# Kernel optimization log

Measured on AMD Instinct MI355X. Metric: run time of the kernel, lower is better.

Reference implementation:

```python
import jax, jax.numpy as jnp
import numpy as np

B, DIM, H, W = 1, 96, 192, 192
HEADS = 6
HD = DIM // HEADS
WIN = (8, 4)
STRIDE = (4, 2)
WH, WW = WIN
N = WH * WW
SCALE = HD ** -0.5
EPS = 1e-8

_hs = np.arange(0, H - WH + 1, STRIDE[0])
_ws = np.arange(0, W - WW + 1, STRIDE[1])
NH, NW = len(_hs), len(_ws)
HIDX = jnp.asarray(_hs[:, None] + np.arange(WH)[None, :])  # (NH, WH)
WIDX = jnp.asarray(_ws[:, None] + np.arange(WW)[None, :])  # (NW, WW)

# relative-position index table (N, N)
_co = np.stack(np.meshgrid(np.arange(WH), np.arange(WW), indexing='ij')).reshape(2, -1)
_rp = _co[:, :, None] - _co[:, None, :]
_rp[0] += WH - 1
_rp[1] += WW - 1
_rp[0] *= 2 * WW - 1
REL_IDX = jnp.asarray(_rp[0] + _rp[1])


def _clin(wr, wi, x):
    # complex 1x1 conv as channel matmul
    xr, xi = x.real, x.imag
    yr = jnp.einsum('oc,nchw->nohw', wr, xr) - jnp.einsum('oc,nchw->nohw', wi, xi)
    yi = jnp.einsum('oc,nchw->nohw', wr, xi) + jnp.einsum('oc,nchw->nohw', wi, xr)
    return jax.lax.complex(yr, yi)


def _bn(x, g, b):
    # BatchNorm2d in training mode: batch statistics, biased variance, eps=1e-5
    mu = x.mean(axis=(0, 2, 3), keepdims=True)
    var = ((x - mu) ** 2).mean(axis=(0, 2, 3), keepdims=True)
    return g[None, :, None, None] * (x - mu) * jax.lax.rsqrt(var + 1e-5) + b[None, :, None, None]


def _cbn(x, gr, br, gi, bi):
    return jax.lax.complex(_bn(x.real, gr, br), _bn(x.imag, gi, bi))


def _cgelu(x):
    mag = jnp.abs(x)
    return x * (jax.nn.gelu(mag, approximate=False) / (mag + EPS))


def _heads(t):
    # (Bn, H*D, wh, ww) -> (Bn, H, N, D)
    return t.reshape(-1, HEADS, HD, N).transpose(0, 1, 3, 2)


def reference(x_real, x_imag, qkv_wr, qkv_wi, proj_wr, proj_wi, rel,
              mlp1_wr, mlp1_wi, mlp2_wr, mlp2_wi,
              n1_gr, n1_br, n1_gi, n1_bi, n2_gr, n2_br, n2_gi, n2_bi):
    x = jax.lax.complex(x_real, x_imag)  # (B, C, H, W)

    # unfold: gather overlapping windows -> (B, C, NH, NW, WH, WW)
    xw = x[:, :, HIDX[:, None, :, None], WIDX[None, :, None, :]]
    xw = xw.transpose(0, 2, 3, 1, 4, 5).reshape(B * NH * NW, DIM, WH, WW)

    qkv = _clin(qkv_wr, qkv_wi, xw)
    q, k, v = jnp.split(qkv, 3, axis=1)
    q, k, v = _heads(q), _heads(k), _heads(v)

    attn = jnp.einsum('bhnd,bhmd->bhnm', q, jnp.conj(k)) * SCALE
    bias = rel[:, REL_IDX]  # (HEADS, N, N), real
    attn = attn + bias[None]
    mag = jnp.abs(attn)
    wsm = jax.nn.softmax(mag, axis=-1)
    attn = attn * (wsm / (mag + EPS))  # magnitude-softmax, phase preserved
    out = jnp.einsum('bhnm,bhmd->bhnd', attn, v)
    out = out.transpose(0, 1, 3, 2).reshape(-1, DIM, WH, WW)
    out = _clin(proj_wr, proj_wi, out)

    # fold: scatter-add windows back, then overlap-average
    out = out.reshape(B, NH, NW, DIM, WH, WW).transpose(0, 3, 1, 2, 4, 5)
    folded = jnp.zeros((B, DIM, H, W), jnp.complex64).at[
        :, :, HIDX[:, None, :, None], WIDX[None, :, None, :]].add(out)
    counts = jnp.zeros((H, W), jnp.float32).at[
        HIDX[:, None, :, None], WIDX[None, :, None, :]].add(1.0)
    x_ = folded / (counts + EPS)

    x = _cbn(x + x_, n1_gr, n1_br, n1_gi, n1_bi)
    m = _clin(mlp2_wr, mlp2_wi, _cgelu(_clin(mlp1_wr, mlp1_wi, x)))
    x = _cbn(x + m, n2_gr, n2_br, n2_gi, n2_bi)
    return jnp.stack([x.real, x.imag], axis=0)  # (2, B, C, H, W)


def setup_inputs() -> dict:
    key = jax.random.key(0)
    ks = jax.random.split(key, 11)
    n = lambda k, s: jax.random.normal(k, s, jnp.float32) * 0.02
    return {
        'x_real': jax.random.normal(ks[0], (B, DIM, H, W), jnp.float32),
        'x_imag': jax.random.normal(ks[1], (B, DIM, H, W), jnp.float32),
        'qkv_wr': n(ks[2], (3 * DIM, DIM)), 'qkv_wi': n(ks[3], (3 * DIM, DIM)),
        'proj_wr': n(ks[4], (DIM, DIM)), 'proj_wi': n(ks[5], (DIM, DIM)),
        'rel': n(ks[6], (HEADS, (2 * WH - 1) * (2 * WW - 1))),
        'mlp1_wr': n(ks[7], (4 * DIM, DIM)), 'mlp1_wi': n(ks[8], (4 * DIM, DIM)),
        'mlp2_wr': n(ks[9], (DIM, 4 * DIM)), 'mlp2_wi': n(ks[10], (DIM, 4 * DIM)),
        'n1_gr': jnp.ones(DIM), 'n1_br': jnp.zeros(DIM),
        'n1_gi': jnp.ones(DIM), 'n1_bi': jnp.zeros(DIM),
        'n2_gr': jnp.ones(DIM), 'n2_br': jnp.zeros(DIM),
        'n2_gi': jnp.ones(DIM), 'n2_bi': jnp.zeros(DIM),
    }
```

## Files before the change

### kernel.cpp

```cpp
#include <hip/hip_runtime.h>
#include <hip/hip_bf16.h>
#include <math.h>

#define PIX 36864
#define IMW 192
#define NWIN 4465
#define NWIN_W 95
#define NTASK (NWIN * 6)

typedef short bf16x8 __attribute__((ext_vector_type(8)));
typedef short bf16x4 __attribute__((ext_vector_type(4)));
typedef float floatx4 __attribute__((ext_vector_type(4)));

#if defined(__has_builtin)
#  if __has_builtin(__builtin_amdgcn_rcpf)
#    define RCP(x) __builtin_amdgcn_rcpf(x)
#  endif
#endif
#ifndef RCP
#  define RCP(x) (1.0f / (x))
#endif

__device__ __forceinline__ unsigned short f2bf(float f) {
    __hip_bfloat16 h = __float2bfloat16(f);
    return __builtin_bit_cast(unsigned short, h);
}
__device__ __forceinline__ float bf2f(unsigned short b) {
    union { unsigned u; float f; } v; v.u = ((unsigned)b) << 16;
    return v.f;
}

__device__ __forceinline__ void emit3(
    const float* __restrict__ wr, const float* __restrict__ wi,
    unsigned short* __restrict__ outr, unsigned short* __restrict__ outi,
    unsigned short* __restrict__ outni, int e)
{
    outr[e] = f2bf(wr[e]);
    unsigned short b = f2bf(wi[e]);
    outi[e]  = b;
    outni[e] = b ^ 0x8000;
}

__global__ __launch_bounds__(256) void prep_kernel(
    const float* __restrict__ qwr, const float* __restrict__ qwi,
    const float* __restrict__ pwr, const float* __restrict__ pwi,
    const float* __restrict__ w2r, const float* __restrict__ w2i,
    const float* __restrict__ xr,  const float* __restrict__ xi,
    unsigned short* __restrict__ wq, unsigned short* __restrict__ wp,
    unsigned short* __restrict__ w2, float* __restrict__ ssum,
    unsigned short* __restrict__ dr, unsigned short* __restrict__ di)
{
    int blk = blockIdx.x;
    if (blk < 108)      { emit3(qwr, qwi, wq, wq + 27648, wq + 55296, blk * 256 + threadIdx.x); return; }
    if (blk < 144)      { emit3(pwr, pwi, wp, wp + 9216,  wp + 18432, (blk - 108) * 256 + threadIdx.x); return; }
    if (blk < 288)      { emit3(w2r, w2i, w2, w2 + 36864, w2 + 73728, (blk - 144) * 256 + threadIdx.x); return; }
    if (blk == 288)     { for (int j = threadIdx.x; j < 768; j += 256) ssum[j] = 0.f; return; }
    int e  = blk - 289;
    int kb = e / 144;
    int n  = (e % 144) * 256 + threadIdx.x;
    bf16x8 vr, vi;
#pragma unroll
    for (int j = 0; j < 8; ++j) {
        ((unsigned short*)&vr)[j] = f2bf(xr[(size_t)(kb * 8 + j) * PIX + n]);
        ((unsigned short*)&vi)[j] = f2bf(xi[(size_t)(kb * 8 + j) * PIX + n]);
    }
    *(bf16x8*)&dr[((size_t)kb * PIX + n) * 8] = vr;
    *(bf16x8*)&di[((size_t)kb * PIX + n) * 8] = vi;
}

template<int K, int MT, int STORE>
__global__ __launch_bounds__(256, 2) void cgemm_mfma_kernel(
    const unsigned short* __restrict__ Wr, const unsigned short* __restrict__ Wi,
    const unsigned short* __restrict__ Wni,
    const unsigned short* __restrict__ Xr, const unsigned short* __restrict__ Xi,
    unsigned short* __restrict__ Pr, unsigned short* __restrict__ Pi, int N)
{
    const int lane = threadIdx.x & 63;
    const int wave = threadIdx.x >> 6;
    const int g = lane >> 4;
    const int r = lane & 15;
    const int m0 = (blockIdx.x % MT) * 32;
    const int n0 = (blockIdx.x / MT) * 256 + wave * 64;

    floatx4 accR[2][4], accI[2][4];
#pragma unroll
    for (int t = 0; t < 2; ++t)
#pragma unroll
        for (int j = 0; j < 4; ++j) {
            accR[t][j] = (floatx4){0.f, 0.f, 0.f, 0.f};
            accI[t][j] = (floatx4){0.f, 0.f, 0.f, 0.f};
        }

    for (int kc = 0; kc < K; kc += 32) {
        bf16x8 awr[2], awi[2], awni[2];
#pragma unroll
        for (int t = 0; t < 2; ++t) {
            size_t wb = (size_t)(m0 + t * 16 + r) * K + kc + g * 8;
            awr[t]  = *(const bf16x8*)&Wr[wb];
            awi[t]  = *(const bf16x8*)&Wi[wb];
            awni[t] = *(const bf16x8*)&Wni[wb];
        }
        bf16x8 bxr[4], bxi[4];
        const size_t krow = (size_t)((kc >> 3) + g);
#pragma unroll
        for (int j = 0; j < 4; ++j) {
            size_t off = (krow * N + n0 + j * 16 + r) * 8;
            bxr[j] = *(const bf16x8*)&Xr[off];
            bxi[j] = *(const bf16x8*)&Xi[off];
        }
#pragma unroll
        for (int t = 0; t < 2; ++t)
#pragma unroll
            for (int j = 0; j < 4; ++j) {
                accR[t][j] = __builtin_amdgcn_mfma_f32_16x16x32_bf16(awr[t],  bxr[j], accR[t][j], 0, 0, 0);
                accR[t][j] = __builtin_amdgcn_mfma_f32_16x16x32_bf16(awni[t], bxi[j], accR[t][j], 0, 0, 0);
                accI[t][j] = __builtin_amdgcn_mfma_f32_16x16x32_bf16(awr[t],  bxi[j], accI[t][j], 0, 0, 0);
                accI[t][j] = __builtin_amdgcn_mfma_f32_16x16x32_bf16(awi[t],  bxr[j], accI[t][j], 0, 0, 0);
            }
    }

    if (STORE == 3) {
#pragma unroll
        for (int t = 0; t < 2; ++t)
#pragma unroll
            for (int j = 0; j < 4; ++j) {
                int col = n0 + j * 16 + r;
#pragma unroll
                for (int reg = 0; reg < 4; ++reg) {
                    int row = m0 + t * 16 + g * 4 + reg;
                    Pr[(size_t)row * N + col] = f2bf(accR[t][j][reg]);
                    Pi[(size_t)row * N + col] = f2bf(accI[t][j][reg]);
                }
            }
    } else {
#pragma unroll
        for (int t = 0; t < 2; ++t) {
            int ch0 = m0 + t * 16;
            int which = ch0 / 96;
            int hh = (ch0 % 96) / 16;
#pragma unroll
            for (int j = 0; j < 4; ++j) {
                int col = n0 + j * 16 + r;
                bf16x4 pr, pi;
#pragma unroll
                for (int reg = 0; reg < 4; ++reg) {
                    ((unsigned short*)&pr)[reg] = f2bf(accR[t][j][reg]);
                    ((unsigned short*)&pi)[reg] = f2bf(accI[t][j][reg]);
                }
                size_t sb = (((size_t)col * 3 + which) * 6 + hh) * 32;
                *(bf16x4*)&Pr[sb + g * 4]      = pr;
                *(bf16x4*)&Pr[sb + 16 + g * 4] = pi;
            }
        }
    }
}

__global__ __launch_bounds__(256) void attn_mfma_kernel(
    const unsigned short* __restrict__ qkvb,
    const float* __restrict__ rel,
    unsigned short* __restrict__ wout)
{
    __shared__ unsigned aLDS[4][32 * 36];
    __shared__ unsigned vLDS[4][32 * 17];

    const int wv   = threadIdx.x >> 6;
    const int lane = threadIdx.x & 63;
    const int lr   = lane & 15;
    const int g    = lane >> 4;

    int t = blockIdx.x * 4 + wv;
    if (t >= NTASK) t = NTASK - 1;
    const int w = t / 6, h = t % 6;
    const int nh = w / NWIN_W, nw = w % NWIN_W;
    const int r0 = nh * 4, c0 = nw * 2;
    const int slot = ((nh & 1) << 1) | (nw & 1);

    unsigned* AL = aLDS[wv];
    unsigned* VL = vLDS[wv];

    auto slotq = [&](int p, int which) -> size_t {
        int gpix = (r0 + (p >> 2)) * IMW + c0 + (p & 3);
        return ((size_t)gpix * 18 + which * 6 + h) * 32;
    };

    {
        int m = lane & 31;
        int half = lane >> 5;
        size_t sv = slotq(m, 2);
        const bf16x8 vr = *(const bf16x8*)&qkvb[sv + half * 8];
        const bf16x8 vi = *(const bf16x8*)&qkvb[sv + 16 + half * 8];
#pragma unroll
        for (int j = 0; j < 8; ++j) {
            unsigned pk = (unsigned)(unsigned short)vr[j] |
                          ((unsigned)(unsigned short)vi[j] << 16);
            VL[m * 17 + half * 8 + j] = pk;
        }
    }

    const int hoff = (g >> 1) * 16;
    const int loff = (g & 1) * 8;
    const unsigned sm = (g >= 2) ? 0x80008000u : 0u;
    bf16x8 Are[2], Aim[2], Bre[2], Bim[2];
#pragma unroll
    for (int tt = 0; tt < 2; ++tt) {
        size_t sq = slotq(tt * 16 + lr, 0);
        size_t sk = slotq(tt * 16 + lr, 1);
        Are[tt] = *(const bf16x8*)&qkvb[sq + hoff + loff];
        Aim[tt] = *(const bf16x8*)&qkvb[sq + (16 - hoff) + loff];
        Bre[tt] = *(const bf16x8*)&qkvb[sk + hoff + loff];
        bf16x8 tmp = Bre[tt];
        unsigned* u = (unsigned*)&tmp;
        u[0] ^= sm; u[1] ^= sm; u[2] ^= sm; u[3] ^= sm;
        Bim[tt] = tmp;
    }

    const floatx4 z4 = (floatx4){0.f, 0.f, 0.f, 0.f};
    floatx4 Sre[2][2], Sim[2][2];
#pragma unroll
    for (int tn = 0; tn < 2; ++tn)
#pragma unroll
        for (int tm = 0; tm < 2; ++tm) {
            Sre[tn][tm] = __builtin_amdgcn_mfma_f32_16x16x32_bf16(Are[tn], Bre[tm], z4, 0, 0, 0);
            Sim[tn][tm] = __builtin_amdgcn_mfma_f32_16x16x32_bf16(Aim[tn], Bim[tm], z4, 0, 0, 0);
        }

    const float* relh = rel + h * 105;
#pragma unroll
    for (int tn = 0; tn < 2; ++tn)
#pragma unroll
        for (int tm = 0; tm < 2; ++tm) {
            int m = tm * 16 + lr;
            int ym = m >> 2, xm = m & 3;
            int yn = tn * 4 + g;
            int bidx = (yn - ym + 7) * 7 + (3 - xm);
#pragma unroll
            for (int reg = 0; reg < 4; ++reg) {
                float re = Sre[tn][tm][reg] * 0.25f + relh[bidx + reg];
                float im = Sim[tn][tm][reg] * 0.25f;
                int n = tn * 16 + g * 4 + reg;
                AL[n * 36 + m] = (unsigned)f2bf(re) | ((unsigned)f2bf(im) << 16);
            }
        }
    __syncthreads();

    {
        const int row = lane & 31;
        const int half = lane >> 5;
        unsigned* rp = &AL[row * 36 + half * 16];
        unsigned pk[16];
        *(uint4*)&pk[0]  = *(const uint4*)&rp[0];
        *(uint4*)&pk[4]  = *(const uint4*)&rp[4];
        *(uint4*)&pk[8]  = *(const uint4*)&rp[8];
        *(uint4*)&pk[12] = *(const uint4*)&rp[12];
        float re[16], im[16], mg[16], rr[16];
#pragma unroll
        for (int j = 0; j < 16; ++j) {
            union { unsigned u; float f; } a, b;
            a.u = pk[j] << 16;
            b.u = pk[j] & 0xffff0000u;
            re[j] = a.f; im[j] = b.f;
            float m2 = fmaf(a.f, a.f, b.f * b.f);
            float rv = rsqrtf(m2 + 1e-16f);
            rr[j] = rv;
            mg[j] = m2 * rv;
        }
        float mx = mg[0];
#pragma unroll
        for (int j = 1; j < 16; ++j) mx = fmaxf(mx, mg[j]);
        mx = fmaxf(mx, __shfl_xor(mx, 32, 64));
        float es[16], ss = 0.f;
#pragma unroll
        for (int j = 0; j < 16; ++j) { es[j] = __expf(mg[j] - mx); ss += es[j]; }
        ss += __shfl_xor(ss, 32, 64);
        float inv = RCP(ss);
#pragma unroll
        for (int j = 0; j < 16; ++j) {
            float f = es[j] * inv * rr[j];
            pk[j] = (unsigned)f2bf(re[j] * f) | ((unsigned)f2bf(im[j] * f) << 16);
        }
        *(uint4*)&rp[0]  = *(uint4*)&pk[0];
        *(uint4*)&rp[4]  = *(uint4*)&pk[4];
        *(uint4*)&rp[8]  = *(uint4*)&pk[8];
        *(uint4*)&rp[12] = *(uint4*)&pk[12];
    }
    __syncthreads();

    floatx4 Pre[2] = {z4, z4}, Pim[2] = {z4, z4};
#pragma unroll
    for (int kc = 0; kc < 2; ++kc) {
        bf16x8 Bpr, Bpi;
        unsigned* bpr = (unsigned*)&Bpr;
        unsigned* bpi = (unsigned*)&Bpi;
#pragma unroll
        for (int p = 0; p < 4; ++p) {
            unsigned pv = VL[(kc * 16 + g * 4 + p) * 17 + lr];
            bpr[p] = pv ^ 0x80000000u;
            bpi[p] = (pv >> 16) | (pv << 16);
        }
#pragma unroll
        for (int tn = 0; tn < 2; ++tn) {
            bf16x8 Af = *(bf16x8*)&AL[(tn * 16 + lr) * 36 + kc * 16 + g * 4];
            Pre[tn] = __builtin_amdgcn_mfma_f32_16x16x32_bf16(Af, Bpr, Pre[tn], 0, 0, 0);
            Pim[tn] = __builtin_amdgcn_mfma_f32_16x16x32_bf16(Af, Bpi, Pim[tn], 0, 0, 0);
        }
    }

#pragma unroll
    for (int tn = 0; tn < 2; ++tn)
#pragma unroll
        for (int reg = 0; reg < 4; ++reg) {
            int n = tn * 16 + g * 4 + reg;
            int gpix = (r0 + (n >> 2)) * IMW + c0 + (n & 3);
            int ch = h * 16 + lr;
            unsigned pk = (unsigned)f2bf(Pre[tn][reg]) |
                          ((unsigned)f2bf(Pim[tn][reg]) << 16);
            *(unsigned*)&wout[(((size_t)gpix * 4 + slot) * 96 + ch) * 2] = pk;
        }
}

__global__ __launch_bounds__(256) void fold_pack_kernel(
    const unsigned short* __restrict__ wout,
    unsigned short* __restrict__ dr, unsigned short* __restrict__ di)
{
    int e = blockIdx.x * 256 + threadIdx.x;
    int gpix = e / 12;
    int kb   = e % 12;
    int r = gpix / IMW, c = gpix % IMW;
    int nh0 = (r >= 7) ? ((r - 4) >> 2) : 0;
    int nh1 = min(46, r >> 2);
    int nw0 = (c >= 3) ? ((c - 2) >> 1) : 0;
    int nw1 = min(94, c >> 1);

    float accr[8] = {0,0,0,0,0,0,0,0}, acci[8] = {0,0,0,0,0,0,0,0};
    int cnt = 0;
    for (int nh = nh0; nh <= nh1; ++nh)
        for (int nw = nw0; nw <= nw1; ++nw) {
            int slot = ((nh & 1) << 1) | (nw & 1);
            const unsigned short* src = &wout[(((size_t)gpix * 4 + slot) * 96 + kb * 8) * 2];
            bf16x8 a = *(const bf16x8*)&src[0];
            bf16x8 b = *(const bf16x8*)&src[8];
#pragma unroll
            for (int j = 0; j < 4; ++j) {
                accr[j]     += bf2f((unsigned short)a[j*2]);
                acci[j]     += bf2f((unsigned short)a[j*2+1]);
                accr[4 + j] += bf2f((unsigned short)b[j*2]);
                acci[4 + j] += bf2f((unsigned short)b[j*2+1]);
            }
            ++cnt;
        }
    float invc = 1.0f / ((float)cnt + 1e-8f);
    bf16x8 pr, pi;
#pragma unroll
    for (int j = 0; j < 8; ++j) {
        ((unsigned short*)&pr)[j] = f2bf(accr[j] * invc);
        ((unsigned short*)&pi)[j] = f2bf(acci[j] * invc);
    }
    *(bf16x8*)&dr[((size_t)kb * PIX + gpix) * 8] = pr;
    *(bf16x8*)&di[((size_t)kb * PIX + gpix) * 8] = pi;
}

__device__ __forceinline__ void reduce32_commit(
    float* st, int kb, float* __restrict__ ssum)
{
#pragma unroll
    for (int v = 0; v < 32; ++v)
#pragma unroll
        for (int msk = 1; msk < 64; msk <<= 1)
            st[v] += __shfl_xor(st[v], msk, 64);
    __shared__ float red[4][32];
    const int wv = threadIdx.x >> 6;
    if ((threadIdx.x & 63) == 0)
#pragma unroll
        for (int v = 0; v < 32; ++v) red[wv][v] = st[v];
    __syncthreads();
    if (threadIdx.x < 32) {
        float s = red[0][threadIdx.x] + red[1][threadIdx.x] +
                  red[2][threadIdx.x] + red[3][threadIdx.x];
        int ch = kb * 8 + (threadIdx.x >> 2);
        int stat = threadIdx.x & 3;
        int base = (stat < 2) ? ch : 96 + ch;
        atomicAdd(&ssum[base * 2 + (stat & 1)], s);
    }
}

__global__ __launch_bounds__(256) void combine_pack_kernel(
    const float* __restrict__ xr, const float* __restrict__ xi,
    const unsigned short* __restrict__ pr, const unsigned short* __restrict__ pi,
    unsigned short* __restrict__ dr, unsigned short* __restrict__ di,
    float* __restrict__ ssum)
{
    const int kb = blockIdx.x / 36;
    const int pb = blockIdx.x % 36;
    const int p0 = pb * 1024;
    float st[32];
#pragma unroll
    for (int v = 0; v < 32; ++v) st[v] = 0.f;

#pragma unroll
    for (int it = 0; it < 4; ++it) {
        int p = p0 + it * 256 + threadIdx.x;
        bf16x8 vr, vi;
#pragma unroll
        for (int ch = 0; ch < 8; ++ch) {
            int c = kb * 8 + ch;
            float a = xr[(size_t)c * PIX + p] + bf2f(pr[(size_t)c * PIX + p]);
            float b = xi[(size_t)c * PIX + p] + bf2f(pi[(size_t)c * PIX + p]);
            ((unsigned short*)&vr)[ch] = f2bf(a);
            ((unsigned short*)&vi)[ch] = f2bf(b);
            st[ch * 4 + 0] += a; st[ch * 4 + 1] += a * a;
            st[ch * 4 + 2] += b; st[ch * 4 + 3] += b * b;
        }
        *(bf16x8*)&dr[((size_t)kb * PIX + p) * 8] = vr;
        *(bf16x8*)&di[((size_t)kb * PIX + p) * 8] = vi;
    }
    reduce32_commit(st, kb, ssum);
}

__global__ __launch_bounds__(256) void scale_w_kernel(
    const float* __restrict__ w1r, const float* __restrict__ w1i,
    const float* __restrict__ gr, const float* __restrict__ br,
    const float* __restrict__ gi, const float* __restrict__ bi,
    const float* __restrict__ ssum1,
    unsigned short* __restrict__ W0, unsigned short* __restrict__ W1,
    unsigned short* __restrict__ W2, unsigned short* __restrict__ W3,
    float* __restrict__ biasR, float* __restrict__ biasI)
{
    const float invn = 1.0f / (float)PIX;
    int blk = blockIdx.x;
    if (blk < 576) {
        int e = blk * 256 + threadIdx.x;
        int mat = e / 36864;
        int idx = e % 36864;
        int k = idx % 96;
        float mr = ssum1[k * 2] * invn;
        float a_r = gr[k] * rsqrtf(ssum1[k * 2 + 1] * invn - mr * mr + 1e-5f);
        float mi = ssum1[(96 + k) * 2] * invn;
        float a_i = gi[k] * rsqrtf(ssum1[(96 + k) * 2 + 1] * invn - mi * mi + 1e-5f);
        float wr = w1r[idx], wi = w1i[idx];
        float v = (mat == 0) ? wr * a_r : (mat == 1) ? -wi * a_i
                : (mat == 2) ? wr * a_i : wi * a_r;
        unsigned short* dst = (mat == 0) ? W0 : (mat == 1) ? W1 : (mat == 2) ? W2 : W3;
        dst[idx] = f2bf(v);
    } else {
        int o = (blk - 576) * 256 + threadIdx.x;
        if (o >= 768) return;
        int isI = o >= 384;
        int oo = o % 384;
        float acc = 0.f;
        for (int k = 0; k < 96; ++k) {
            float mr = ssum1[k * 2] * invn;
            float a_r = gr[k] * rsqrtf(ssum1[k * 2 + 1] * invn - mr * mr + 1e-5f);
            float c_r = br[k] - a_r * mr;
            float mi = ssum1[(96 + k) * 2] * invn;
            float a_i = gi[k] * rsqrtf(ssum1[(96 + k) * 2 + 1] * invn - mi * mi + 1e-5f);
            float c_i = bi[k] - a_i * mi;
            float wr = w1r[oo * 96 + k], wi = w1i[oo * 96 + k];
            acc += isI ? (wr * c_i + wi * c_r) : (wr * c_r - wi * c_i);
        }
        (isI ? biasI : biasR)[oo] = acc;
    }
}

__global__ __launch_bounds__(256, 2) void mlp1bn_kernel(
    const unsigned short* __restrict__ W0, const unsigned short* __restrict__ W1,
    const unsigned short* __restrict__ W2, const unsigned short* __restrict__ W3,
    const float* __restrict__ biasR, const float* __restrict__ biasI,
    const unsigned short* __restrict__ Xr, const unsigned short* __restrict__ Xi,
    unsigned short* __restrict__ Pr, unsigned short* __restrict__ Pi, int N)
{
    const int lane = threadIdx.x & 63;
    const int wave = threadIdx.x >> 6;
    const int g = lane >> 4;
    const int r = lane & 15;
    const int m0 = (blockIdx.x % 12) * 32;
    const int n0 = (blockIdx.x / 12) * 256 + wave * 64;
    const int K = 96;

    floatx4 accR[2][4], accI[2][4];
#pragma unroll
    for (int t = 0; t < 2; ++t)
#pragma unroll
        for (int j = 0; j < 4; ++j) {
            accR[t][j] = (floatx4){0.f, 0.f, 0.f, 0.f};
            accI[t][j] = (floatx4){0.f, 0.f, 0.f, 0.f};
        }

    for (int kc = 0; kc < K; kc += 32) {
        bf16x8 a0[2], a1[2], a2[2], a3[2];
#pragma unroll
        for (int t = 0; t < 2; ++t) {
            size_t wb = (size_t)(m0 + t * 16 + r) * K + kc + g * 8;
            a0[t] = *(const bf16x8*)&W0[wb];
            a1[t] = *(const bf16x8*)&W1[wb];
            a2[t] = *(const bf16x8*)&W2[wb];
            a3[t] = *(const bf16x8*)&W3[wb];
        }
        bf16x8 bxr[4], bxi[4];
        const size_t krow = (size_t)((kc >> 3) + g);
#pragma unroll
        for (int j = 0; j < 4; ++j) {
            size_t off = (krow * N + n0 + j * 16 + r) * 8;
            bxr[j] = *(const bf16x8*)&Xr[off];
            bxi[j] = *(const bf16x8*)&Xi[off];
        }
#pragma unroll
        for (int t = 0; t < 2; ++t)
#pragma unroll
            for (int j = 0; j < 4; ++j) {
                accR[t][j] = __builtin_amdgcn_mfma_f32_16x16x32_bf16(a0[t], bxr[j], accR[t][j], 0, 0, 0);
                accR[t][j] = __builtin_amdgcn_mfma_f32_16x16x32_bf16(a1[t], bxi[j], accR[t][j], 0, 0, 0);
                accI[t][j] = __builtin_amdgcn_mfma_f32_16x16x32_bf16(a2[t], bxi[j], accI[t][j], 0, 0, 0);
                accI[t][j] = __builtin_amdgcn_mfma_f32_16x16x32_bf16(a3[t], bxr[j], accI[t][j], 0, 0, 0);
            }
    }

#pragma unroll
    for (int t = 0; t < 2; ++t) {
        float bR[4], bI[4];
#pragma unroll
        for (int reg = 0; reg < 4; ++reg) {
            int row = m0 + t * 16 + g * 4 + reg;
            bR[reg] = biasR[row];
            bI[reg] = biasI[row];
        }
#pragma unroll
        for (int j = 0; j < 4; ++j) {
            int col = n0 + j * 16 + r;
            size_t rowblk = (size_t)((m0 + t * 16 + g * 4) >> 3);
            int sub = (g & 1) * 4;
            bf16x4 pr, pi;
#pragma unroll
            for (int reg = 0; reg < 4; ++reg) {
                float a = accR[t][j][reg] + bR[reg];
                float b = accI[t][j][reg] + bI[reg];
                float m2 = fmaf(a, a, b * b);
                float rv = rsqrtf(m2 + 1e-16f);
                float mag = m2 * rv;
                float f = (0.5f + 0.5f * erff(mag * 0.70710678118654752f)) * mag * rv;
                ((unsigned short*)&pr)[reg] = f2bf(a * f);
                ((unsigned short*)&pi)[reg] = f2bf(b * f);
            }
            *(bf16x4*)&Pr[(rowblk * N + col) * 8 + sub] = pr;
            *(bf16x4*)&Pi[(rowblk * N + col) * 8 + sub] = pi;
        }
    }
}

__global__ __launch_bounds__(256) void addbn_kernel(
    const unsigned short* __restrict__ dr, const unsigned short* __restrict__ di,
    const float* __restrict__ ssum1,
    const float* __restrict__ gr, const float* __restrict__ br,
    const float* __restrict__ gi, const float* __restrict__ bi,
    const unsigned short* __restrict__ mr_, const unsigned short* __restrict__ mi_,
    unsigned short* __restrict__ s2r, unsigned short* __restrict__ s2i,
    float* __restrict__ ssum2)
{
    const int kb = blockIdx.x / 36;
    const int pb = blockIdx.x % 36;
    const int p0 = pb * 1024;
    const float invn = 1.0f / (float)PIX;

    float ar[8], cr[8], ai[8], ci[8];
#pragma unroll
    for (int ch = 0; ch < 8; ++ch) {
        int c = kb * 8 + ch;
        float mr = ssum1[c * 2] * invn;
        ar[ch] = gr[c] * rsqrtf(ssum1[c * 2 + 1] * invn - mr * mr + 1e-5f);
        cr[ch] = br[c] - ar[ch] * mr;
        float mi = ssum1[(96 + c) * 2] * invn;
        ai[ch] = gi[c] * rsqrtf(ssum1[(96 + c) * 2 + 1] * invn - mi * mi + 1e-5f);
        ci[ch] = bi[c] - ai[ch] * mi;
    }

    float st[32];
#pragma unroll
    for (int v = 0; v < 32; ++v) st[v] = 0.f;

#pragma unroll
    for (int it = 0; it < 4; ++it) {
        int p = p0 + it * 256 + threadIdx.x;
        bf16x8 s1r = *(const bf16x8*)&dr[((size_t)kb * PIX + p) * 8];
        bf16x8 s1i = *(const bf16x8*)&di[((size_t)kb * PIX + p) * 8];
#pragma unroll
        for (int ch = 0; ch < 8; ++ch) {
            int c = kb * 8 + ch;
            float vr = bf2f(mr_[(size_t)c * PIX + p]) + ar[ch] * bf2f((unsigned short)s1r[ch]) + cr[ch];
            float vi = bf2f(mi_[(size_t)c * PIX + p]) + ai[ch] * bf2f((unsigned short)s1i[ch]) + ci[ch];
            s2r[(size_t)c * PIX + p] = f2bf(vr);
            s2i[(size_t)c * PIX + p] = f2bf(vi);
            st[ch * 4 + 0] += vr; st[ch * 4 + 1] += vr * vr;
            st[ch * 4 + 2] += vi; st[ch * 4 + 3] += vi * vi;
        }
    }
    reduce32_commit(st, kb, ssum2);
}

__global__ __launch_bounds__(256) void bn_apply_kernel(
    const unsigned short* __restrict__ s2r, const unsigned short* __restrict__ s2i,
    const float* __restrict__ gr, const float* __restrict__ br,
    const float* __restrict__ gi, const float* __restrict__ bi,
    const float* __restrict__ ssum2,
    float* __restrict__ outr, float* __restrict__ outi)
{
    int e = blockIdx.x * 256 + threadIdx.x;
    if (e >= 96 * PIX) return;
    int ch = e / PIX;
    const float invn = 1.0f / (float)PIX;
    float mr = ssum2[ch * 2] * invn;
    float isr = rsqrtf(ssum2[ch * 2 + 1] * invn - mr * mr + 1e-5f);
    float mi = ssum2[(96 + ch) * 2] * invn;
    float isi = rsqrtf(ssum2[(96 + ch) * 2 + 1] * invn - mi * mi + 1e-5f);
    outr[e] = gr[ch] * (bf2f(s2r[e]) - mr) * isr + br[ch];
    outi[e] = gi[ch] * (bf2f(s2i[e]) - mi) * isi + bi[ch];
}

extern "C" void kernel_launch(void* const* d_in, const int* in_sizes, int n_in,
                              void* d_out, int out_size, void* d_ws, size_t ws_size,
                              hipStream_t stream)
{
    const float* x_r     = (const float*)d_in[0];
    const float* x_i     = (const float*)d_in[1];
    const float* qkv_wr  = (const float*)d_in[2];
    const float* qkv_wi  = (const float*)d_in[3];
    const float* proj_wr = (const float*)d_in[4];
    const float* proj_wi = (const float*)d_in[5];
    const float* rel     = (const float*)d_in[6];
    const float* mlp1_wr = (const float*)d_in[7];
    const float* mlp1_wi = (const float*)d_in[8];
    const float* mlp2_wr = (const float*)d_in[9];
    const float* mlp2_wi = (const float*)d_in[10];
    const float* n1_gr   = (const float*)d_in[11];
    const float* n1_br   = (const float*)d_in[12];
    const float* n1_gi   = (const float*)d_in[13];
    const float* n1_bi   = (const float*)d_in[14];
    const float* n2_gr   = (const float*)d_in[15];
    const float* n2_br   = (const float*)d_in[16];
    const float* n2_gi   = (const float*)d_in[17];
    const float* n2_bi   = (const float*)d_in[18];

    const size_t P = PIX;
    char* base = (char*)d_ws;

    unsigned short* Dr = (unsigned short*)base;
    unsigned short* Di = Dr + 96 * P;
    char* R = (char*)(Di + 96 * P);
    unsigned short* qkvb = (unsigned short*)R;
    unsigned short* wout = qkvb + 576 * P;
    unsigned short* pm_r = (unsigned short*)R;
    unsigned short* pm_i = pm_r + 96 * P;
    unsigned short* hid_r = pm_i + 96 * P;
    unsigned short* hid_i = hid_r + 384 * P;
    unsigned short* Wb = wout + (size_t)P * 4 * 96 * 2;

    unsigned short* wq = Wb;
    unsigned short* wp = Wb + 82944;
    unsigned short* w2 = Wb + 110592;
    unsigned short* W1s = Wb + 221184;
    float* biasR = (float*)(Wb + 368640);
    float* biasI = biasR + 384;
    float* ssum1 = biasI + 384;
    float* ssum2 = ssum1 + 384;
    unsigned short* s2r = (unsigned short*)(ssum2 + 384);
    unsigned short* s2i = s2r + 96 * P;

    float* out_r = (float*)d_out;
    float* out_i = out_r + 96 * P;

    dim3 blk(256);

    prep_kernel<<<dim3(2017), blk, 0, stream>>>(
        qkv_wr, qkv_wi, proj_wr, proj_wi, mlp2_wr, mlp2_wi, x_r, x_i,
        wq, wp, w2, ssum1, Dr, Di);
    cgemm_mfma_kernel<96, 9, 2><<<dim3(9 * 144), blk, 0, stream>>>(
        wq, wq + 27648, wq + 55296, Dr, Di, qkvb, nullptr, PIX);
    attn_mfma_kernel<<<dim3((NTASK + 3) / 4), blk, 0, stream>>>(qkvb, rel, wout);
    fold_pack_kernel<<<dim3(1728), blk, 0, stream>>>(wout, Dr, Di);
    cgemm_mfma_kernel<96, 3, 3><<<dim3(3 * 144), blk, 0, stream>>>(
        wp, wp + 9216, wp + 18432, Dr, Di, pm_r, pm_i, PIX);
    combine_pack_kernel<<<dim3(432), blk, 0, stream>>>(x_r, x_i, pm_r, pm_i, Dr, Di, ssum1);
    scale_w_kernel<<<dim3(579), blk, 0, stream>>>(
        mlp1_wr, mlp1_wi, n1_gr, n1_br, n1_gi, n1_bi, ssum1,
        W1s, W1s + 36864, W1s + 73728, W1s + 110592, biasR, biasI);
    mlp1bn_kernel<<<dim3(12 * 144), blk, 0, stream>>>(
        W1s, W1s + 36864, W1s + 73728, W1s + 110592, biasR, biasI,
        Dr, Di, hid_r, hid_i, PIX);
    cgemm_mfma_kernel<384, 3, 3><<<dim3(3 * 144), blk, 0, stream>>>(
        w2, w2 + 36864, w2 + 73728, hid_r, hid_i, pm_r, pm_i, PIX);
    addbn_kernel<<<dim3(432), blk, 0, stream>>>(Dr, Di, ssum1,
        n1_gr, n1_br, n1_gi, n1_bi, pm_r, pm_i, s2r, s2i, ssum2);
    bn_apply_kernel<<<dim3(13824), blk, 0, stream>>>(s2r, s2i,
        n2_gr, n2_br, n2_gi, n2_bi, ssum2, out_r, out_i);
}
```

Before: 332.4 us.

## Compute transposed scores to keep softmax and PV operands in registers

Swaps the operand roles in the QK^T MFMA so the score tiles come out transposed, with each lane holding a row fragment that lines up with the A-operand layout of the PV MFMA. Softmax is done directly on the accumulator registers, using cross-lane shuffles for the row max and sum, and the result is packed straight into bf16x8 operands. This removes the per-wave LDS scratch buffer for the attention matrix, its store/load round trip and one barrier. In exchange it adds extra shuffles and more register pressure, which is only one part of a multi-kernel pipeline.

```diff
diff --git a/kernel.cpp b/kernel.cpp
--- a/kernel.cpp
+++ b/kernel.cpp
@@ -160,7 +160,6 @@
     const float* __restrict__ rel,
     unsigned short* __restrict__ wout)
 {
-    __shared__ unsigned aLDS[4][32 * 36];
     __shared__ unsigned vLDS[4][32 * 17];
 
     const int wv   = threadIdx.x >> 6;
@@ -175,7 +174,6 @@
     const int r0 = nh * 4, c0 = nw * 2;
     const int slot = ((nh & 1) << 1) | (nw & 1);
 
-    unsigned* AL = aLDS[wv];
     unsigned* VL = vLDS[wv];
 
     auto slotq = [&](int p, int which) -> size_t {
@@ -199,89 +197,70 @@
 
     const int hoff = (g >> 1) * 16;
     const int loff = (g & 1) * 8;
-    const unsigned sm = (g >= 2) ? 0x80008000u : 0u;
-    bf16x8 Are[2], Aim[2], Bre[2], Bim[2];
+    const unsigned smq = (g < 2) ? 0x80008000u : 0u;
+    bf16x8 AkRe[2], AkIm[2], BqRe[2], BqIm[2];
 #pragma unroll
     for (int tt = 0; tt < 2; ++tt) {
         size_t sq = slotq(tt * 16 + lr, 0);
         size_t sk = slotq(tt * 16 + lr, 1);
-        Are[tt] = *(const bf16x8*)&qkvb[sq + hoff + loff];
-        Aim[tt] = *(const bf16x8*)&qkvb[sq + (16 - hoff) + loff];
-        Bre[tt] = *(const bf16x8*)&qkvb[sk + hoff + loff];
-        bf16x8 tmp = Bre[tt];
+        AkRe[tt] = *(const bf16x8*)&qkvb[sk + hoff + loff];
+        AkIm[tt] = *(const bf16x8*)&qkvb[sk + (16 - hoff) + loff];
+        BqRe[tt] = *(const bf16x8*)&qkvb[sq + hoff + loff];
+        bf16x8 tmp = BqRe[tt];
         unsigned* u = (unsigned*)&tmp;
-        u[0] ^= sm; u[1] ^= sm; u[2] ^= sm; u[3] ^= sm;
-        Bim[tt] = tmp;
+        u[0] ^= smq; u[1] ^= smq; u[2] ^= smq; u[3] ^= smq;
+        BqIm[tt] = tmp;
     }
 
     const floatx4 z4 = (floatx4){0.f, 0.f, 0.f, 0.f};
     floatx4 Sre[2][2], Sim[2][2];
 #pragma unroll
-    for (int tn = 0; tn < 2; ++tn)
-#pragma unroll
-        for (int tm = 0; tm < 2; ++tm) {
-            Sre[tn][tm] = __builtin_amdgcn_mfma_f32_16x16x32_bf16(Are[tn], Bre[tm], z4, 0, 0, 0);
-            Sim[tn][tm] = __builtin_amdgcn_mfma_f32_16x16x32_bf16(Aim[tn], Bim[tm], z4, 0, 0, 0);
+    for (int tm = 0; tm < 2; ++tm)
+#pragma unroll
+        for (int tn = 0; tn < 2; ++tn) {
+            Sre[tm][tn] = __builtin_amdgcn_mfma_f32_16x16x32_bf16(AkRe[tm], BqRe[tn], z4, 0, 0, 0);
+            Sim[tm][tn] = __builtin_amdgcn_mfma_f32_16x16x32_bf16(AkIm[tm], BqIm[tn], z4, 0, 0, 0);
         }
 
     const float* relh = rel + h * 105;
-#pragma unroll
-    for (int tn = 0; tn < 2; ++tn)
-#pragma unroll
-        for (int tm = 0; tm < 2; ++tm) {
-            int m = tm * 16 + lr;
-            int ym = m >> 2, xm = m & 3;
-            int yn = tn * 4 + g;
-            int bidx = (yn - ym + 7) * 7 + (3 - xm);
+    bf16x8 pa[2][2];
+#pragma unroll
+    for (int tn = 0; tn < 2; ++tn) {
+        float re8[8], im8[8], mg8[8], rr8[8];
+#pragma unroll
+        for (int tm = 0; tm < 2; ++tm)
 #pragma unroll
             for (int reg = 0; reg < 4; ++reg) {
-                float re = Sre[tn][tm][reg] * 0.25f + relh[bidx + reg];
-                float im = Sim[tn][tm][reg] * 0.25f;
-                int n = tn * 16 + g * 4 + reg;
-                AL[n * 36 + m] = (unsigned)f2bf(re) | ((unsigned)f2bf(im) << 16);
-            }
-        }
-    __syncthreads();
-
-    {
-        const int row = lane & 31;
-        const int half = lane >> 5;
-        unsigned* rp = &AL[row * 36 + half * 16];
-        unsigned pk[16];
-        *(uint4*)&pk[0]  = *(const uint4*)&rp[0];
-        *(uint4*)&pk[4]  = *(const uint4*)&rp[4];
-        *(uint4*)&pk[8]  = *(const uint4*)&rp[8];
-        *(uint4*)&pk[12] = *(const uint4*)&rp[12];
-        float re[16], im[16], mg[16], rr[16];
-#pragma unroll
-        for (int j = 0; j < 16; ++j) {
-            union { unsigned u; float f; } a, b;
-            a.u = pk[j] << 16;
-            b.u = pk[j] & 0xffff0000u;
-            re[j] = a.f; im[j] = b.f;
-            float m2 = fmaf(a.f, a.f, b.f * b.f);
-            float rv = rsqrtf(m2 + 1e-16f);
-            rr[j] = rv;
-            mg[j] = m2 * rv;
-        }
-        float mx = mg[0];
-#pragma unroll
-        for (int j = 1; j < 16; ++j) mx = fmaxf(mx, mg[j]);
+                int j = tm * 4 + reg;
+                int bidx = ((tn * 4 + (lr >> 2)) - (tm * 4 + g) + 7) * 7 + ((lr & 3) - reg + 3);
+                float re = Sre[tm][tn][reg] * 0.25f + relh[bidx];
+                float im = Sim[tm][tn][reg] * 0.25f;
+                re8[j] = re; im8[j] = im;
+                float m2 = fmaf(re, re, im * im);
+                float rv = rsqrtf(m2 + 1e-16f);
+                rr8[j] = rv;
+                mg8[j] = m2 * rv;
+            }
+        float mx = mg8[0];
+#pragma unroll
+        for (int j = 1; j < 8; ++j) mx = fmaxf(mx, mg8[j]);
+        mx = fmaxf(mx, __shfl_xor(mx, 16, 64));
         mx = fmaxf(mx, __shfl_xor(mx, 32, 64));
-        float es[16], ss = 0.f;
-#pragma unroll
-        for (int j = 0; j < 16; ++j) { es[j] = __expf(mg[j] - mx); ss += es[j]; }
+        float es8[8], ss = 0.f;
+#pragma unroll
+        for (int j = 0; j < 8; ++j) { es8[j] = __expf(mg8[j] - mx); ss += es8[j]; }
+        ss += __shfl_xor(ss, 16, 64);
         ss += __shfl_xor(ss, 32, 64);
         float inv = RCP(ss);
 #pragma unroll
-        for (int j = 0; j < 16; ++j) {
-            float f = es[j] * inv * rr[j];
-            pk[j] = (unsigned)f2bf(re[j] * f) | ((unsigned)f2bf(im[j] * f) << 16);
-        }
-        *(uint4*)&rp[0]  = *(uint4*)&pk[0];
-        *(uint4*)&rp[4]  = *(uint4*)&pk[4];
-        *(uint4*)&rp[8]  = *(uint4*)&pk[8];
-        *(uint4*)&rp[12] = *(uint4*)&pk[12];
+        for (int tm = 0; tm < 2; ++tm)
+#pragma unroll
+            for (int reg = 0; reg < 4; ++reg) {
+                int j = tm * 4 + reg;
+                float f = es8[j] * inv * rr8[j];
+                ((unsigned short*)&pa[tn][tm])[reg * 2]     = f2bf(re8[j] * f);
+                ((unsigned short*)&pa[tn][tm])[reg * 2 + 1] = f2bf(im8[j] * f);
+            }
     }
     __syncthreads();
 
@@ -299,9 +278,8 @@
         }
 #pragma unroll
         for (int tn = 0; tn < 2; ++tn) {
-            bf16x8 Af = *(bf16x8*)&AL[(tn * 16 + lr) * 36 + kc * 16 + g * 4];
-            Pre[tn] = __builtin_amdgcn_mfma_f32_16x16x32_bf16(Af, Bpr, Pre[tn], 0, 0, 0);
-            Pim[tn] = __builtin_amdgcn_mfma_f32_16x16x32_bf16(Af, Bpi, Pim[tn], 0, 0, 0);
+            Pre[tn] = __builtin_amdgcn_mfma_f32_16x16x32_bf16(pa[tn][kc], Bpr, Pre[tn], 0, 0, 0);
+            Pim[tn] = __builtin_amdgcn_mfma_f32_16x16x32_bf16(pa[tn][kc], Bpi, Pim[tn], 0, 0, 0);
         }
     }
 
```

Result: no change. 328.6 us (-1.1%).
